# Kernel tuning notes

Measured on AMD Instinct MI355X. Metric: run time of the kernel, lower is better.

## Reference

```python
import jax, jax.numpy as jnp
import numpy as np

B, S, D, H = 2, 2048, 1024, 16
HD = D // H  # head dim = 64


def setup_inputs() -> dict:
    key = jax.random.key(0)
    ks = jax.random.split(key, 5)
    scale = 1.0 / np.sqrt(D)
    return {
        "hidden_states": jax.random.normal(ks[0], (B, S, D), jnp.float32),
        "attention_mask": jax.random.normal(ks[1], (B, 1, 1, S), jnp.float32),
        "Wq": jax.random.normal(ks[2], (D, D), jnp.float32) * scale,
        "bq": jnp.zeros((D,), jnp.float32),
        "Wk": jax.random.normal(ks[3], (D, D), jnp.float32) * scale,
        "bk": jnp.zeros((D,), jnp.float32),
        "Wv": jax.random.normal(ks[4], (D, D), jnp.float32) * scale,
        "bv": jnp.zeros((D,), jnp.float32),
    }


def _split_heads(x):
    # [B,S,D] -> [B,H,S,HD]
    return x.reshape(B, S, H, HD).transpose(0, 2, 1, 3)


def reference(hidden_states, attention_mask, Wq, bq, Wk, bk, Wv, bv):
    # torch Linear: y = x @ W.T + b
    q = _split_heads(hidden_states @ Wq.T + bq)
    k = _split_heads(hidden_states @ Wk.T + bk)
    v = _split_heads(hidden_states @ Wv.T + bv)

    scores = jnp.einsum("bhqd,bhkd->bhqk", q, k)
    # Faithful to source: with a mask present, the 1/sqrt(head_dim) scaling
    # is overwritten and raw scores are multiplied by the binary key mask.
    mask = (attention_mask >= 0).astype(scores.dtype)  # [B,1,1,S]
    probs = scores * mask
    # dropout prob = 0 (eval) -> identity

    ctx = jnp.einsum("bhqk,bhkd->bhqd", probs, v)
    ctx = ctx.transpose(0, 2, 1, 3).reshape(B, S, D)
    return ctx
```

## Files before the change

kernel.cpp:

```cpp
#include <hip/hip_runtime.h>

#define BB 2
#define SS 2048
#define DD 1024
#define HH 16
#define HDIM 64
#define MTOT 4096

typedef unsigned short u16;
typedef __bf16 bf16_t;
typedef bf16_t bf16x8 __attribute__((ext_vector_type(8)));
typedef float floatx4 __attribute__((ext_vector_type(4)));
typedef float floatx16 __attribute__((ext_vector_type(16)));

__device__ __forceinline__ float bf2f(u16 u) {
  union { unsigned int i; float f; } x;
  x.i = ((unsigned int)u) << 16;
  return x.f;
}
__device__ __forceinline__ u16 f2bf(float f) {
  union { float f; unsigned int i; } x;
  x.f = f;
  unsigned int r = x.i + 0x7fffu + ((x.i >> 16) & 1u);
  return (u16)(r >> 16);
}

__device__ __forceinline__ void gload16(const u16* g, u16* l) {
  __builtin_amdgcn_global_load_lds(
      (const __attribute__((address_space(1))) unsigned int*)g,
      (__attribute__((address_space(3))) unsigned int*)l, 16, 0, 0);
}

__global__ __launch_bounds__(256) void cast_to_bf16(
    const float* __restrict__ hs, const float* __restrict__ wq,
    const float* __restrict__ wk, const float* __restrict__ wv,
    u16* __restrict__ hs_b, u16* __restrict__ wq_b,
    u16* __restrict__ wk_b, u16* __restrict__ wv_b) {
  int fid = blockIdx.x * 256 + threadIdx.x;
  const float* src;
  u16* dst;
  int local;
  if (fid < 1048576) { src = hs; dst = hs_b; local = fid; }
  else if (fid < 1310720) { src = wq; dst = wq_b; local = fid - 1048576; }
  else if (fid < 1572864) { src = wk; dst = wk_b; local = fid - 1310720; }
  else { src = wv; dst = wv_b; local = fid - 1572864; }
  float4 v = reinterpret_cast<const float4*>(src)[local];
  ushort4 o;
  o.x = f2bf(v.x); o.y = f2bf(v.y); o.z = f2bf(v.z); o.w = f2bf(v.w);
  reinterpret_cast<ushort4*>(dst)[local] = o;
}

#define BKK 32
__global__ __launch_bounds__(256) void qkv_gemm_kernel(
    const u16* __restrict__ A,
    const u16* __restrict__ Wq, const u16* __restrict__ Wk, const u16* __restrict__ Wv,
    const float* __restrict__ bq, const float* __restrict__ bk, const float* __restrict__ bv,
    u16* __restrict__ Qo, u16* __restrict__ Ko, u16* __restrict__ Vo) {
  __shared__ u16 sA[128 * BKK];
  __shared__ u16 sB[128 * BKK];
  const int mt = blockIdx.y, ntall = blockIdx.x;
  const int seg = ntall >> 3, nt = ntall & 7;
  const u16* Wp = (seg == 0) ? Wq : (seg == 1) ? Wk : Wv;
  const float* bp = (seg == 0) ? bq : (seg == 1) ? bk : bv;
  u16* Out = (seg == 0) ? Qo : (seg == 1) ? Ko : Vo;
  const int m0 = mt * 128, n0 = nt * 128;
  const int tid = threadIdx.x;
  const int lane = tid & 63, wave = tid >> 6;
  const int wm = (wave >> 1) * 64, wn = (wave & 1) * 64;
  const int l32 = lane & 31, khalf = lane >> 5;
  const int srow0 = wave * 32 + (lane >> 2);
  const int scol = (lane & 3) * 8;
  floatx16 acc[2][2] = {};
  for (int k0 = 0; k0 < DD; k0 += BKK) {
#pragma unroll
    for (int c = 0; c < 2; ++c) {
      int r = srow0 + c * 16;
      gload16(A + (size_t)(m0 + r) * DD + k0 + scol, sA + r * BKK + scol);
      gload16(Wp + (size_t)(n0 + r) * DD + k0 + scol, sB + r * BKK + scol);
    }
    __syncthreads();
#pragma unroll
    for (int kk = 0; kk < 2; ++kk) {
      bf16x8 af[2], bfr[2];
#pragma unroll
      for (int i = 0; i < 2; ++i)
        af[i] = *reinterpret_cast<const bf16x8*>(sA + (wm + i * 32 + l32) * BKK + kk * 16 + khalf * 8);
#pragma unroll
      for (int j = 0; j < 2; ++j)
        bfr[j] = *reinterpret_cast<const bf16x8*>(sB + (wn + j * 32 + l32) * BKK + kk * 16 + khalf * 8);
#pragma unroll
      for (int i = 0; i < 2; ++i)
#pragma unroll
        for (int j = 0; j < 2; ++j)
          acc[i][j] = __builtin_amdgcn_mfma_f32_32x32x16_bf16(af[i], bfr[j], acc[i][j], 0, 0, 0);
    }
    __syncthreads();
  }
#pragma unroll
  for (int j = 0; j < 2; ++j) {
    int col = n0 + wn + j * 32 + l32;
    float bias = bp[col];
#pragma unroll
    for (int i = 0; i < 2; ++i) {
#pragma unroll
      for (int reg = 0; reg < 16; ++reg) {
        int row = m0 + wm + i * 32 + (reg & 3) + 8 * (reg >> 2) + 4 * khalf;
        Out[(size_t)row * DD + col] = f2bf(acc[i][j][reg] + bias);
      }
    }
  }
}

__global__ __launch_bounds__(256) void m_partial_kernel(
    const u16* __restrict__ Xb, const u16* __restrict__ Yb,
    const float* __restrict__ am, float* __restrict__ mpart) {
  __shared__ float sX[64 * 68];
  __shared__ float sY[64 * 68];
  const int bh = blockIdx.y;
  const int b = bh >> 4, h = bh & 15;
  const int tid = threadIdx.x;
  const int e0 = (tid & 15) * 4, d0 = (tid >> 4) * 4;
  const int s0 = blockIdx.x * 64;
  float acc[4][4] = {};
#pragma unroll
  for (int c = 0; c < 2; ++c) {
    int L = tid + c * 256;
    int srow = L >> 3;
    int col = (L & 7) * 8;
    size_t g = (size_t)(b * SS + s0 + srow) * DD + h * HDIM + col;
    uint4 xraw = *reinterpret_cast<const uint4*>(Xb + g);
    uint4 yraw = *reinterpret_cast<const uint4*>(Yb + g);
    float m = (am[b * SS + s0 + srow] >= 0.f) ? 1.f : 0.f;
    unsigned int xw[4] = {xraw.x, xraw.y, xraw.z, xraw.w};
    unsigned int yw[4] = {yraw.x, yraw.y, yraw.z, yraw.w};
#pragma unroll
    for (int q = 0; q < 4; ++q) {
      sX[srow * 68 + col + 2 * q]     = m * bf2f((u16)(xw[q] & 0xffffu));
      sX[srow * 68 + col + 2 * q + 1] = m * bf2f((u16)(xw[q] >> 16));
      sY[srow * 68 + col + 2 * q]     = bf2f((u16)(yw[q] & 0xffffu));
      sY[srow * 68 + col + 2 * q + 1] = bf2f((u16)(yw[q] >> 16));
    }
  }
  __syncthreads();
  for (int s = 0; s < 64; ++s) {
    float4 xx = *reinterpret_cast<const float4*>(&sX[s * 68 + e0]);
    float4 yy = *reinterpret_cast<const float4*>(&sY[s * 68 + d0]);
    float xa[4] = {xx.x, xx.y, xx.z, xx.w};
    float ya[4] = {yy.x, yy.y, yy.z, yy.w};
#pragma unroll
    for (int i = 0; i < 4; ++i)
#pragma unroll
      for (int j = 0; j < 4; ++j) acc[i][j] += xa[i] * ya[j];
  }
  float* outp = mpart + ((size_t)(blockIdx.x * 32 + bh)) * 4096;
#pragma unroll
  for (int i = 0; i < 4; ++i) {
    float4 o = {acc[i][0], acc[i][1], acc[i][2], acc[i][3]};
    *reinterpret_cast<float4*>(&outp[(e0 + i) * 64 + d0]) = o;
  }
}

__global__ __launch_bounds__(128) void m_reduce_kernel(
    const float* __restrict__ mpart, u16* __restrict__ Mb) {
  int t = blockIdx.x * 128 + threadIdx.x;
  const float* p = mpart + (size_t)t * 4;
  float4 s = {0.f, 0.f, 0.f, 0.f};
#pragma unroll
  for (int pc = 0; pc < 32; ++pc) {
    float4 v = *reinterpret_cast<const float4*>(p + (size_t)pc * 131072);
    s.x += v.x; s.y += v.y; s.z += v.z; s.w += v.w;
  }
  ushort4 o = {f2bf(s.x), f2bf(s.y), f2bf(s.z), f2bf(s.w)};
  *reinterpret_cast<ushort4*>(Mb + (size_t)t * 4) = o;
}

__global__ __launch_bounds__(256) void ctx_kernel(
    const u16* __restrict__ Qb, const u16* __restrict__ Mb, float* __restrict__ Out) {
  __shared__ u16 sMT[64 * 72];
  const int m0 = blockIdx.x * 128;
  const int h = blockIdx.y;
  const int b = m0 >> 11;
  const int bh = b * HH + h;
  const int tid = threadIdx.x;
  const u16* mg = Mb + (size_t)bh * 4096;
#pragma unroll
  for (int c = 0; c < 2; ++c) {
    int L = c * 256 + tid;
    int d = L >> 3, e = (L & 7) * 8;
    *reinterpret_cast<uint4*>(&sMT[d * 72 + e]) =
        *reinterpret_cast<const uint4*>(&mg[d * 64 + e]);
  }
  __syncthreads();
  const int lane = tid & 63, wave = tid >> 6;
  const int l32 = lane & 31, khalf = lane >> 5;
  const int arow = m0 + wave * 32 + l32;
  const u16* qrow = Qb + (size_t)arow * DD + h * HDIM + khalf * 8;
  bf16x8 af[4], bfr[2][4];
#pragma unroll
  for (int k0 = 0; k0 < 4; ++k0) {
    af[k0] = *reinterpret_cast<const bf16x8*>(qrow + k0 * 16);
#pragma unroll
    for (int j = 0; j < 2; ++j)
      bfr[j][k0] = *reinterpret_cast<const bf16x8*>(
          &sMT[(j * 32 + l32) * 72 + k0 * 16 + khalf * 8]);
  }
  floatx16 acc[2] = {};
#pragma unroll
  for (int j = 0; j < 2; ++j)
#pragma unroll
    for (int k0 = 0; k0 < 4; ++k0)
      acc[j] = __builtin_amdgcn_mfma_f32_32x32x16_bf16(af[k0], bfr[j][k0], acc[j], 0, 0, 0);
#pragma unroll
  for (int j = 0; j < 2; ++j) {
    int col = h * HDIM + j * 32 + l32;
#pragma unroll
    for (int reg = 0; reg < 16; ++reg) {
      int r = m0 + wave * 32 + (reg & 3) + 8 * (reg >> 2) + 4 * khalf;
      Out[(size_t)r * DD + col] = acc[j][reg];
    }
  }
}

extern "C" void kernel_launch(void* const* d_in, const int* in_sizes, int n_in,
                              void* d_out, int out_size, void* d_ws, size_t ws_size,
                              hipStream_t stream) {
  const float* hs = (const float*)d_in[0];
  const float* am = (const float*)d_in[1];
  const float* wq = (const float*)d_in[2];
  const float* bq = (const float*)d_in[3];
  const float* wk = (const float*)d_in[4];
  const float* bk = (const float*)d_in[5];
  const float* wv = (const float*)d_in[6];
  const float* bv = (const float*)d_in[7];
  float* out = (float*)d_out;
  char* ws = (char*)d_ws;

  u16* hs_b = (u16*)(ws);
  u16* wq_b = (u16*)(ws + 8388608);
  u16* wk_b = (u16*)(ws + 10485760);
  u16* wv_b = (u16*)(ws + 12582912);
  u16* q_b  = (u16*)(ws + 14680064);
  u16* k_b  = (u16*)(ws + 23068672);
  u16* v_b  = (u16*)(ws + 31457280);
  float* mpart = (float*)(ws + 39845888);
  u16* m_b  = (u16*)(ws + 56623104);

  cast_to_bf16<<<7168, 256, 0, stream>>>(hs, wq, wk, wv, hs_b, wq_b, wk_b, wv_b);
  qkv_gemm_kernel<<<dim3(24, 32), 256, 0, stream>>>(hs_b, wq_b, wk_b, wv_b,
                                                    bq, bk, bv, q_b, k_b, v_b);
  m_partial_kernel<<<dim3(32, 32), 256, 0, stream>>>(v_b, k_b, am, mpart);
  m_reduce_kernel<<<256, 128, 0, stream>>>(mpart, m_b);
  ctx_kernel<<<dim3(32, 16), 256, 0, stream>>>(q_b, m_b, out);
}
```

Before: 147.5 us.

## Double-buffer QKV GEMM LDS tiles, XOR-swizzle layout, and remap block order

The QKV projection GEMM now keeps two LDS buffers and issues the global-to-LDS loads for the next K tile before computing on the current one, so memory latency can overlap with MFMA work. LDS columns are XOR-swizzled by row to reduce bank conflicts on the fragment reads. Block indices are also remapped so neighbouring blocks share A/W tiles in cache. The cost is double the LDS footprint per block, which may lower occupancy.

```diff
diff --git a/kernel.cpp b/kernel.cpp
--- a/kernel.cpp
+++ b/kernel.cpp
@@ -56,9 +56,11 @@
     const u16* __restrict__ Wq, const u16* __restrict__ Wk, const u16* __restrict__ Wv,
     const float* __restrict__ bq, const float* __restrict__ bk, const float* __restrict__ bv,
     u16* __restrict__ Qo, u16* __restrict__ Ko, u16* __restrict__ Vo) {
-  __shared__ u16 sA[128 * BKK];
-  __shared__ u16 sB[128 * BKK];
-  const int mt = blockIdx.y, ntall = blockIdx.x;
+  __shared__ u16 sA[2][128 * BKK];
+  __shared__ u16 sB[2][128 * BKK];
+  const int d = blockIdx.y * 24 + blockIdx.x;
+  const int swz = (d & 7) * 96 + (d >> 3);
+  const int mt = swz / 24, ntall = swz % 24;
   const int seg = ntall >> 3, nt = ntall & 7;
   const u16* Wp = (seg == 0) ? Wq : (seg == 1) ? Wk : Wv;
   const float* bp = (seg == 0) ? bq : (seg == 1) ? bk : bv;
@@ -69,25 +71,43 @@
   const int wm = (wave >> 1) * 64, wn = (wave & 1) * 64;
   const int l32 = lane & 31, khalf = lane >> 5;
   const int srow0 = wave * 32 + (lane >> 2);
-  const int scol = (lane & 3) * 8;
+  const int slot = lane & 3;
+
+#define STAGE(buf, kbase)                                                    \
+  {                                                                          \
+    _Pragma("unroll") for (int c = 0; c < 2; ++c) {                          \
+      int r = srow0 + c * 16;                                                \
+      int gc = ((slot ^ (r & 3)) * 8);       \
+      gload16(A + (size_t)(m0 + r) * DD + (kbase) + gc,                      \
+              &sA[buf][r * BKK + slot * 8]);                                 \
+      gload16(Wp + (size_t)(n0 + r) * DD + (kbase) + gc,                     \
+              &sB[buf][r * BKK + slot * 8]);                                 \
+    }                                                                        \
+  }
+
   floatx16 acc[2][2] = {};
-  for (int k0 = 0; k0 < DD; k0 += BKK) {
-#pragma unroll
-    for (int c = 0; c < 2; ++c) {
-      int r = srow0 + c * 16;
-      gload16(A + (size_t)(m0 + r) * DD + k0 + scol, sA + r * BKK + scol);
-      gload16(Wp + (size_t)(n0 + r) * DD + k0 + scol, sB + r * BKK + scol);
-    }
-    __syncthreads();
+  STAGE(0, 0);
+  __syncthreads();
+  for (int t = 0; t < 32; ++t) {
+    const int cur = t & 1;
+    if (t < 31) STAGE(cur ^ 1, (t + 1) * BKK);
+    const u16* pA = sA[cur];
+    const u16* pB = sB[cur];
 #pragma unroll
     for (int kk = 0; kk < 2; ++kk) {
       bf16x8 af[2], bfr[2];
 #pragma unroll
-      for (int i = 0; i < 2; ++i)
-        af[i] = *reinterpret_cast<const bf16x8*>(sA + (wm + i * 32 + l32) * BKK + kk * 16 + khalf * 8);
-#pragma unroll
-      for (int j = 0; j < 2; ++j)
-        bfr[j] = *reinterpret_cast<const bf16x8*>(sB + (wn + j * 32 + l32) * BKK + kk * 16 + khalf * 8);
+      for (int i = 0; i < 2; ++i) {
+        int ra = wm + i * 32 + l32;
+        af[i] = *reinterpret_cast<const bf16x8*>(
+            pA + ra * BKK + (((kk * 2 + khalf) ^ (ra & 3)) * 8));
+      }
+#pragma unroll
+      for (int j = 0; j < 2; ++j) {
+        int rb = wn + j * 32 + l32;
+        bfr[j] = *reinterpret_cast<const bf16x8*>(
+            pB + rb * BKK + (((kk * 2 + khalf) ^ (rb & 3)) * 8));
+      }
 #pragma unroll
       for (int i = 0; i < 2; ++i)
 #pragma unroll
@@ -96,6 +116,7 @@
     }
     __syncthreads();
   }
+#undef STAGE
 #pragma unroll
   for (int j = 0; j < 2; ++j) {
     int col = n0 + wn + j * 32 + l32;
```

Measured after the change: 145.8 us. No clear change (-1.2%).

## Fuse all five stages into one cooperative kernel with grid syncs

Applied to the files above, without the earlier changes.

Replaces the five separate launches (cast, QKV GEMM, partial K^T V, reduce, ctx GEMM) with a single cooperative kernel of 768 blocks that runs each stage in turn, separated by grid-wide syncs. The aim is to remove per-launch overhead and the idle gaps between kernels. In exchange, every stage is tied to a fixed grid of 768 blocks at 3 blocks per CU, so stages that would like more or fewer blocks get less parallelism, and each grid sync adds its own cost. If the cooperative launch fails, the code falls back to the original five launches.

```diff
diff --git a/kernel.cpp b/kernel.cpp
--- a/kernel.cpp
+++ b/kernel.cpp
@@ -1,4 +1,7 @@
 #include <hip/hip_runtime.h>
+#include <hip/hip_cooperative_groups.h>
+
+namespace cg = cooperative_groups;
 
 #define BB 2
 #define SS 2048
@@ -6,6 +9,9 @@
 #define HH 16
 #define HDIM 64
 #define MTOT 4096
+#define BKK 32
+#define NBLK 768
+#define NTHR 196608
 
 typedef unsigned short u16;
 typedef __bf16 bf16_t;
@@ -29,6 +35,198 @@
   __builtin_amdgcn_global_load_lds(
       (const __attribute__((address_space(1))) unsigned int*)g,
       (__attribute__((address_space(3))) unsigned int*)l, 16, 0, 0);
+}
+
+__global__ __launch_bounds__(256, 3) void fused_kernel(
+    const float* __restrict__ hs, const float* __restrict__ am,
+    const float* __restrict__ wq, const float* __restrict__ bq,
+    const float* __restrict__ wk, const float* __restrict__ bk,
+    const float* __restrict__ wv, const float* __restrict__ bv,
+    float* __restrict__ out,
+    u16* __restrict__ hs_b, u16* __restrict__ wq_b,
+    u16* __restrict__ wk_b, u16* __restrict__ wv_b,
+    u16* __restrict__ q_b, u16* __restrict__ k_b, u16* __restrict__ v_b,
+    float* __restrict__ mpart, u16* __restrict__ m_b) {
+  cg::grid_group gg = cg::this_grid();
+  __shared__ __align__(16) char smem[34816];
+  const int tid = threadIdx.x;
+  const int bid = blockIdx.x;
+  const int gtid = bid * 256 + tid;
+  const int lane = tid & 63, wave = tid >> 6;
+  const int l32 = lane & 31, khalf = lane >> 5;
+
+  for (int fid = gtid; fid < 1835008; fid += NTHR) {
+    const float* src; u16* dst; int local;
+    if (fid < 1048576) { src = hs; dst = hs_b; local = fid; }
+    else if (fid < 1310720) { src = wq; dst = wq_b; local = fid - 1048576; }
+    else if (fid < 1572864) { src = wk; dst = wk_b; local = fid - 1310720; }
+    else { src = wv; dst = wv_b; local = fid - 1572864; }
+    float4 v = reinterpret_cast<const float4*>(src)[local];
+    ushort4 o;
+    o.x = f2bf(v.x); o.y = f2bf(v.y); o.z = f2bf(v.z); o.w = f2bf(v.w);
+    reinterpret_cast<ushort4*>(dst)[local] = o;
+  }
+  gg.sync();
+
+  {
+    u16* sA = reinterpret_cast<u16*>(smem);
+    u16* sB = reinterpret_cast<u16*>(smem + 8192);
+    const int mt = bid / 24, ntall = bid % 24;
+    const int seg = ntall >> 3, nt = ntall & 7;
+    const u16* Wp = (seg == 0) ? wq_b : (seg == 1) ? wk_b : wv_b;
+    const float* bp = (seg == 0) ? bq : (seg == 1) ? bk : bv;
+    u16* Out = (seg == 0) ? q_b : (seg == 1) ? k_b : v_b;
+    const int m0 = mt * 128, n0 = nt * 128;
+    const int wm = (wave >> 1) * 64, wn = (wave & 1) * 64;
+    const int srow0 = wave * 32 + (lane >> 2);
+    const int scol = (lane & 3) * 8;
+    floatx16 acc[2][2] = {};
+    for (int k0 = 0; k0 < DD; k0 += BKK) {
+#pragma unroll
+      for (int c = 0; c < 2; ++c) {
+        int r = srow0 + c * 16;
+        gload16(hs_b + (size_t)(m0 + r) * DD + k0 + scol, sA + r * BKK + scol);
+        gload16(Wp + (size_t)(n0 + r) * DD + k0 + scol, sB + r * BKK + scol);
+      }
+      __syncthreads();
+#pragma unroll
+      for (int kk = 0; kk < 2; ++kk) {
+        bf16x8 af[2], bfr[2];
+#pragma unroll
+        for (int i = 0; i < 2; ++i)
+          af[i] = *reinterpret_cast<const bf16x8*>(sA + (wm + i * 32 + l32) * BKK + kk * 16 + khalf * 8);
+#pragma unroll
+        for (int j = 0; j < 2; ++j)
+          bfr[j] = *reinterpret_cast<const bf16x8*>(sB + (wn + j * 32 + l32) * BKK + kk * 16 + khalf * 8);
+#pragma unroll
+        for (int i = 0; i < 2; ++i)
+#pragma unroll
+          for (int j = 0; j < 2; ++j)
+            acc[i][j] = __builtin_amdgcn_mfma_f32_32x32x16_bf16(af[i], bfr[j], acc[i][j], 0, 0, 0);
+      }
+      __syncthreads();
+    }
+#pragma unroll
+    for (int j = 0; j < 2; ++j) {
+      int col = n0 + wn + j * 32 + l32;
+      float bias = bp[col];
+#pragma unroll
+      for (int i = 0; i < 2; ++i) {
+#pragma unroll
+        for (int reg = 0; reg < 16; ++reg) {
+          int row = m0 + wm + i * 32 + (reg & 3) + 8 * (reg >> 2) + 4 * khalf;
+          Out[(size_t)row * DD + col] = f2bf(acc[i][j][reg] + bias);
+        }
+      }
+    }
+  }
+  gg.sync();
+
+  {
+    float* sX = reinterpret_cast<float*>(smem);
+    float* sY = reinterpret_cast<float*>(smem + 17408);
+    const int e0 = (tid & 15) * 4, d0 = (tid >> 4) * 4;
+    for (int vb = bid; vb < 1024; vb += NBLK) {
+      const int chunk = vb >> 5, bh = vb & 31;
+      const int b = bh >> 4, h = bh & 15;
+      const int s0 = chunk * 64;
+      if (vb != bid) __syncthreads();
+      float acc[4][4] = {};
+#pragma unroll
+      for (int c = 0; c < 2; ++c) {
+        int L = tid + c * 256;
+        int srow = L >> 3;
+        int col = (L & 7) * 8;
+        size_t g = (size_t)(b * SS + s0 + srow) * DD + h * HDIM + col;
+        uint4 xraw = *reinterpret_cast<const uint4*>(v_b + g);
+        uint4 yraw = *reinterpret_cast<const uint4*>(k_b + g);
+        float m = (am[b * SS + s0 + srow] >= 0.f) ? 1.f : 0.f;
+        unsigned int xw[4] = {xraw.x, xraw.y, xraw.z, xraw.w};
+        unsigned int yw[4] = {yraw.x, yraw.y, yraw.z, yraw.w};
+#pragma unroll
+        for (int q = 0; q < 4; ++q) {
+          sX[srow * 68 + col + 2 * q]     = m * bf2f((u16)(xw[q] & 0xffffu));
+          sX[srow * 68 + col + 2 * q + 1] = m * bf2f((u16)(xw[q] >> 16));
+          sY[srow * 68 + col + 2 * q]     = bf2f((u16)(yw[q] & 0xffffu));
+          sY[srow * 68 + col + 2 * q + 1] = bf2f((u16)(yw[q] >> 16));
+        }
+      }
+      __syncthreads();
+      for (int s = 0; s < 64; ++s) {
+        float4 xx = *reinterpret_cast<const float4*>(&sX[s * 68 + e0]);
+        float4 yy = *reinterpret_cast<const float4*>(&sY[s * 68 + d0]);
+        float xa[4] = {xx.x, xx.y, xx.z, xx.w};
+        float ya[4] = {yy.x, yy.y, yy.z, yy.w};
+#pragma unroll
+        for (int i = 0; i < 4; ++i)
+#pragma unroll
+          for (int j = 0; j < 4; ++j) acc[i][j] += xa[i] * ya[j];
+      }
+      float* outp = mpart + ((size_t)(chunk * 32 + bh)) * 4096;
+#pragma unroll
+      for (int i = 0; i < 4; ++i) {
+        float4 o = {acc[i][0], acc[i][1], acc[i][2], acc[i][3]};
+        *reinterpret_cast<float4*>(&outp[(e0 + i) * 64 + d0]) = o;
+      }
+    }
+  }
+  gg.sync();
+
+  if (gtid < 32768) {
+    const float* p = mpart + (size_t)gtid * 4;
+    float4 s = {0.f, 0.f, 0.f, 0.f};
+#pragma unroll
+    for (int pc = 0; pc < 32; ++pc) {
+      float4 v = *reinterpret_cast<const float4*>(p + (size_t)pc * 131072);
+      s.x += v.x; s.y += v.y; s.z += v.z; s.w += v.w;
+    }
+    ushort4 o = {f2bf(s.x), f2bf(s.y), f2bf(s.z), f2bf(s.w)};
+    *reinterpret_cast<ushort4*>(m_b + (size_t)gtid * 4) = o;
+  }
+  gg.sync();
+
+  if (bid < 512) {
+    u16* sMT = reinterpret_cast<u16*>(smem);
+    const int mtile = bid & 31, h = bid >> 5;
+    const int m0 = mtile * 128;
+    const int b = m0 >> 11;
+    const int bh = b * HH + h;
+    const u16* mg = m_b + (size_t)bh * 4096;
+#pragma unroll
+    for (int c = 0; c < 2; ++c) {
+      int L = c * 256 + tid;
+      int d = L >> 3, e = (L & 7) * 8;
+      *reinterpret_cast<uint4*>(&sMT[d * 72 + e]) =
+          *reinterpret_cast<const uint4*>(&mg[d * 64 + e]);
+    }
+    __syncthreads();
+    const int arow = m0 + wave * 32 + l32;
+    const u16* qrow = q_b + (size_t)arow * DD + h * HDIM + khalf * 8;
+    bf16x8 af[4], bfr[2][4];
+#pragma unroll
+    for (int k0 = 0; k0 < 4; ++k0) {
+      af[k0] = *reinterpret_cast<const bf16x8*>(qrow + k0 * 16);
+#pragma unroll
+      for (int j = 0; j < 2; ++j)
+        bfr[j][k0] = *reinterpret_cast<const bf16x8*>(
+            &sMT[(j * 32 + l32) * 72 + k0 * 16 + khalf * 8]);
+    }
+    floatx16 acc[2] = {};
+#pragma unroll
+    for (int j = 0; j < 2; ++j)
+#pragma unroll
+      for (int k0 = 0; k0 < 4; ++k0)
+        acc[j] = __builtin_amdgcn_mfma_f32_32x32x16_bf16(af[k0], bfr[j][k0], acc[j], 0, 0, 0);
+#pragma unroll
+    for (int j = 0; j < 2; ++j) {
+      int col = h * HDIM + j * 32 + l32;
+#pragma unroll
+      for (int reg = 0; reg < 16; ++reg) {
+        int r = m0 + wave * 32 + (reg & 3) + 8 * (reg >> 2) + 4 * khalf;
+        out[(size_t)r * DD + col] = acc[j][reg];
+      }
+    }
+  }
 }
 
 __global__ __launch_bounds__(256) void cast_to_bf16(
@@ -50,7 +248,6 @@
   reinterpret_cast<ushort4*>(dst)[local] = o;
 }
 
-#define BKK 32
 __global__ __launch_bounds__(256) void qkv_gemm_kernel(
     const u16* __restrict__ A,
     const u16* __restrict__ Wq, const u16* __restrict__ Wk, const u16* __restrict__ Wv,
@@ -245,10 +442,19 @@
   float* mpart = (float*)(ws + 39845888);
   u16* m_b  = (u16*)(ws + 56623104);
 
-  cast_to_bf16<<<7168, 256, 0, stream>>>(hs, wq, wk, wv, hs_b, wq_b, wk_b, wv_b);
-  qkv_gemm_kernel<<<dim3(24, 32), 256, 0, stream>>>(hs_b, wq_b, wk_b, wv_b,
-                                                    bq, bk, bv, q_b, k_b, v_b);
-  m_partial_kernel<<<dim3(32, 32), 256, 0, stream>>>(v_b, k_b, am, mpart);
-  m_reduce_kernel<<<256, 128, 0, stream>>>(mpart, m_b);
-  ctx_kernel<<<dim3(32, 16), 256, 0, stream>>>(q_b, m_b, out);
-}
+  void* args[] = {(void*)&hs, (void*)&am, (void*)&wq, (void*)&bq,
+                  (void*)&wk, (void*)&bk, (void*)&wv, (void*)&bv,
+                  (void*)&out, (void*)&hs_b, (void*)&wq_b, (void*)&wk_b,
+                  (void*)&wv_b, (void*)&q_b, (void*)&k_b, (void*)&v_b,
+                  (void*)&mpart, (void*)&m_b};
+  hipError_t err = hipLaunchCooperativeKernel((const void*)fused_kernel,
+                                              dim3(NBLK), dim3(256), args, 0, stream);
+  if (err != hipSuccess) {
+    cast_to_bf16<<<7168, 256, 0, stream>>>(hs, wq, wk, wv, hs_b, wq_b, wk_b, wv_b);
+    qkv_gemm_kernel<<<dim3(24, 32), 256, 0, stream>>>(hs_b, wq_b, wk_b, wv_b,
+                                                      bq, bk, bv, q_b, k_b, v_b);
+    m_partial_kernel<<<dim3(32, 32), 256, 0, stream>>>(v_b, k_b, am, mpart);
+    m_reduce_kernel<<<256, 128, 0, stream>>>(mpart, m_b);
+    ctx_kernel<<<dim3(32, 16), 256, 0, stream>>>(q_b, m_b, out);
+  }
+}
```

Measured after the change: 501.3 us. +239.9%, slower.

## Rewrite QKV GEMM with 256x256 tiles, double-buffered XOR-swizzled LDS, 16x16 MFMA

Applied to the files above, without the earlier changes.

The QKV projection GEMM moves from 128x128 tiles with a single LDS buffer and K-step 32 to 256x256 tiles computed by 512 threads with K-step 64. The next K-slice is prefetched into a second LDS buffer while the current one is consumed, and the LDS layout is XOR-swizzled to avoid bank conflicts. The MFMA shape changes to 16x16x32, the block order is remapped, and MFMA priority is raised with s_setprio. The aim is more operand reuse per byte loaded and overlap of global loads with compute, at the cost of only 192 blocks (fewer than the CU count) and heavy register and LDS use.

```diff
diff --git a/kernel.cpp b/kernel.cpp
--- a/kernel.cpp
+++ b/kernel.cpp
@@ -11,7 +11,6 @@
 typedef __bf16 bf16_t;
 typedef bf16_t bf16x8 __attribute__((ext_vector_type(8)));
 typedef float floatx4 __attribute__((ext_vector_type(4)));
-typedef float floatx16 __attribute__((ext_vector_type(16)));
 
 __device__ __forceinline__ float bf2f(u16 u) {
   union { unsigned int i; float f; } x;
@@ -50,62 +49,98 @@
   reinterpret_cast<ushort4*>(dst)[local] = o;
 }
 
-#define BKK 32
-__global__ __launch_bounds__(256) void qkv_gemm_kernel(
+__global__ __launch_bounds__(512, 2) void qkv_gemm_8ph(
     const u16* __restrict__ A,
     const u16* __restrict__ Wq, const u16* __restrict__ Wk, const u16* __restrict__ Wv,
     const float* __restrict__ bq, const float* __restrict__ bk, const float* __restrict__ bv,
     u16* __restrict__ Qo, u16* __restrict__ Ko, u16* __restrict__ Vo) {
-  __shared__ u16 sA[128 * BKK];
-  __shared__ u16 sB[128 * BKK];
-  const int mt = blockIdx.y, ntall = blockIdx.x;
-  const int seg = ntall >> 3, nt = ntall & 7;
+  __shared__ u16 lds[2][2][16384];
+  const int raw = blockIdx.x;
+  const int id = (raw & 7) * 24 + (raw >> 3);
+  const int seg = id >> 6, rem = id & 63;
+  const int mt = rem >> 2, nt = rem & 3;
   const u16* Wp = (seg == 0) ? Wq : (seg == 1) ? Wk : Wv;
   const float* bp = (seg == 0) ? bq : (seg == 1) ? bk : bv;
   u16* Out = (seg == 0) ? Qo : (seg == 1) ? Ko : Vo;
-  const int m0 = mt * 128, n0 = nt * 128;
+  const int m0 = mt * 256, n0 = nt * 256;
   const int tid = threadIdx.x;
   const int lane = tid & 63, wave = tid >> 6;
-  const int wm = (wave >> 1) * 64, wn = (wave & 1) * 64;
-  const int l32 = lane & 31, khalf = lane >> 5;
-  const int srow0 = wave * 32 + (lane >> 2);
-  const int scol = (lane & 3) * 8;
-  floatx16 acc[2][2] = {};
-  for (int k0 = 0; k0 < DD; k0 += BKK) {
-#pragma unroll
-    for (int c = 0; c < 2; ++c) {
-      int r = srow0 + c * 16;
-      gload16(A + (size_t)(m0 + r) * DD + k0 + scol, sA + r * BKK + scol);
-      gload16(Wp + (size_t)(n0 + r) * DD + k0 + scol, sB + r * BKK + scol);
-    }
-    __syncthreads();
-#pragma unroll
-    for (int kk = 0; kk < 2; ++kk) {
-      bf16x8 af[2], bfr[2];
-#pragma unroll
-      for (int i = 0; i < 2; ++i)
-        af[i] = *reinterpret_cast<const bf16x8*>(sA + (wm + i * 32 + l32) * BKK + kk * 16 + khalf * 8);
-#pragma unroll
-      for (int j = 0; j < 2; ++j)
-        bfr[j] = *reinterpret_cast<const bf16x8*>(sB + (wn + j * 32 + l32) * BKK + kk * 16 + khalf * 8);
-#pragma unroll
-      for (int i = 0; i < 2; ++i)
-#pragma unroll
-        for (int j = 0; j < 2; ++j)
-          acc[i][j] = __builtin_amdgcn_mfma_f32_32x32x16_bf16(af[i], bfr[j], acc[i][j], 0, 0, 0);
-    }
-    __syncthreads();
-  }
-#pragma unroll
-  for (int j = 0; j < 2; ++j) {
-    int col = n0 + wn + j * 32 + l32;
+  const int l15 = lane & 15, kh = lane >> 4;
+  const int wrow0 = (wave >> 2) * 128;
+  const int wcol0 = (wave & 3) * 64;
+
+  int srow[4], sgc[4], soff[4];
+#pragma unroll
+  for (int c = 0; c < 4; ++c) {
+    int L = c * 512 + tid;
+    srow[c] = L >> 3;
+    sgc[c] = ((L & 7) ^ (srow[c] & 7)) << 3;
+    soff[c] = L << 3;
+  }
+
+#define STAGE(buf, kbase)                                                    \
+  {                                                                          \
+    _Pragma("unroll") for (int c = 0; c < 4; ++c) {                          \
+      gload16(A + (size_t)(m0 + srow[c]) * DD + (kbase) + sgc[c],            \
+              &lds[buf][0][soff[c]]);                                        \
+      gload16(Wp + (size_t)(n0 + srow[c]) * DD + (kbase) + sgc[c],           \
+              &lds[buf][1][soff[c]]);                                        \
+    }                                                                        \
+  }
+
+  floatx4 acc[8][4] = {};
+  STAGE(0, 0);
+  asm volatile("s_waitcnt vmcnt(0)" ::: "memory");
+  asm volatile("s_barrier" ::: "memory");
+
+  for (int t = 0; t < 16; ++t) {
+    const int cur = t & 1;
+    const char* pA = (const char*)lds[cur][0];
+    const char* pB = (const char*)lds[cur][1];
+    bf16x8 b[4];
+#pragma unroll
+    for (int p = 0; p < 4; ++p) {
+      const int mg = p & 1, ks = p >> 1;
+      if (p == 0 && t < 15) STAGE(cur ^ 1, (t + 1) * 64);
+      const int sw = (((ks * 4 + kh) ^ (l15 & 7)) << 4);
+      bf16x8 a[4];
+#pragma unroll
+      for (int i = 0; i < 4; ++i) {
+        int ra = wrow0 + (mg * 4 + i) * 16 + l15;
+        a[i] = *reinterpret_cast<const bf16x8*>(pA + ra * 128 + sw);
+      }
+      if (mg == 0) {
+#pragma unroll
+        for (int nf = 0; nf < 4; ++nf) {
+          int rb = wcol0 + nf * 16 + l15;
+          b[nf] = *reinterpret_cast<const bf16x8*>(pB + rb * 128 + sw);
+        }
+      }
+      asm volatile("s_barrier" ::: "memory");
+      __builtin_amdgcn_s_setprio(1);
+#pragma unroll
+      for (int i = 0; i < 4; ++i)
+#pragma unroll
+        for (int nf = 0; nf < 4; ++nf)
+          acc[mg * 4 + i][nf] = __builtin_amdgcn_mfma_f32_16x16x32_bf16(
+              a[i], b[nf], acc[mg * 4 + i][nf], 0, 0, 0);
+      __builtin_amdgcn_s_setprio(0);
+    }
+    asm volatile("s_waitcnt vmcnt(0)" ::: "memory");
+    asm volatile("s_barrier" ::: "memory");
+  }
+#undef STAGE
+
+#pragma unroll
+  for (int nf = 0; nf < 4; ++nf) {
+    int col = n0 + wcol0 + nf * 16 + l15;
     float bias = bp[col];
 #pragma unroll
-    for (int i = 0; i < 2; ++i) {
-#pragma unroll
-      for (int reg = 0; reg < 16; ++reg) {
-        int row = m0 + wm + i * 32 + (reg & 3) + 8 * (reg >> 2) + 4 * khalf;
-        Out[(size_t)row * DD + col] = f2bf(acc[i][j][reg] + bias);
+    for (int mf = 0; mf < 8; ++mf) {
+#pragma unroll
+      for (int j = 0; j < 4; ++j) {
+        int row = m0 + wrow0 + mf * 16 + kh * 4 + j;
+        Out[(size_t)row * DD + col] = f2bf(acc[mf][nf][j] + bias);
       }
     }
   }
@@ -195,6 +230,7 @@
   const int l32 = lane & 31, khalf = lane >> 5;
   const int arow = m0 + wave * 32 + l32;
   const u16* qrow = Qb + (size_t)arow * DD + h * HDIM + khalf * 8;
+  typedef float floatx16 __attribute__((ext_vector_type(16)));
   bf16x8 af[4], bfr[2][4];
 #pragma unroll
   for (int k0 = 0; k0 < 4; ++k0) {
@@ -246,8 +282,8 @@
   u16* m_b  = (u16*)(ws + 56623104);
 
   cast_to_bf16<<<7168, 256, 0, stream>>>(hs, wq, wk, wv, hs_b, wq_b, wk_b, wv_b);
-  qkv_gemm_kernel<<<dim3(24, 32), 256, 0, stream>>>(hs_b, wq_b, wk_b, wv_b,
-                                                    bq, bk, bv, q_b, k_b, v_b);
+  qkv_gemm_8ph<<<192, 512, 0, stream>>>(hs_b, wq_b, wk_b, wv_b,
+                                        bq, bk, bv, q_b, k_b, v_b);
   m_partial_kernel<<<dim3(32, 32), 256, 0, stream>>>(v_b, k_b, am, mpart);
   m_reduce_kernel<<<256, 128, 0, stream>>>(mpart, m_b);
   ctx_kernel<<<dim3(32, 16), 256, 0, stream>>>(q_b, m_b, out);
```

After: 145.1 us. No clear change (-1.6%).
